# Kernel tuning notes

Hardware: AMD Instinct MI355X
Metric: run time of the kernel (lower is better)

## Reference

```python
import jax, jax.numpy as jnp
import numpy as np
from jax import lax

BETA = 0.9   # membrane decay
THR = 1.0    # firing threshold (soft reset)
K = 10       # number of time bins
# spatial pyramid for original_shape=(100,368) under 4 stride-2 SAME convs
HW = [(50, 184), (25, 92), (13, 46), (7, 23)]
CH = [4, 8, 16, 32]


def conv(x, w, b, stride=1):
    y = lax.conv_general_dilated(x, w, (stride, stride), 'SAME',
                                 dimension_numbers=('NCHW', 'OIHW', 'NCHW'))
    return y + b[None, :, None, None]


def spike(u):
    # heaviside forward, sigmoid straight-through surrogate backward
    s = (u > 0.0).astype(u.dtype)
    sg = jax.nn.sigmoid(4.0 * u)
    return sg + lax.stop_gradient(s - sg)


def setup_inputs() -> dict:
    key = jax.random.key(0)
    ks = jax.random.split(key, 12)
    T, B = 1000, 1
    x = jax.random.normal(ks[0], (T, B, 1, 100, 368), jnp.float32)

    def w(k, o, i, kh=3, kw=3):
        return 0.1 * jax.random.normal(k, (o, i, kh, kw), jnp.float32)

    inp = {'x': x}
    cin = [1] + CH[:3]
    for li in range(4):
        inp['w%d' % (li + 1)] = w(ks[1 + li], CH[li], cin[li])
        inp['b%d' % (li + 1)] = jnp.zeros((CH[li],), jnp.float32)
    sc = [2 * K * c for c in CH]  # skip channels: [80,160,320,640]
    inp['dw4'] = w(ks[5], 64, sc[3]); inp['db4'] = jnp.zeros((64,), jnp.float32)
    inp['dw3'] = w(ks[6], 32, 64 + sc[2]); inp['db3'] = jnp.zeros((32,), jnp.float32)
    inp['dw2'] = w(ks[7], 16, 32 + sc[1]); inp['db2'] = jnp.zeros((16,), jnp.float32)
    inp['dw1'] = w(ks[8], 8, 16 + sc[0]); inp['db1'] = jnp.zeros((8,), jnp.float32)
    inp['wo'] = w(ks[9], 1, 8, 1, 1); inp['bo'] = jnp.zeros((1,), jnp.float32)
    inp['total_steps'] = 1000
    inp['block_size'] = 100
    return inp


def reference(x, w1, b1, w2, b2, w3, b3, w4, b4,
              dw4, db4, dw3, db3, dw2, db2, dw1, db1, wo, bo,
              total_steps, block_size):
    S = total_steps // K  # steps per bin
    B = x.shape[1]
    xb = x.reshape((K, S) + x.shape[1:])  # [K,S,B,C,H,W]
    mems0 = tuple(jnp.zeros((B, CH[i], HW[i][0], HW[i][1]), x.dtype) for i in range(4))
    enc_w = [(w1, b1), (w2, b2), (w3, b3), (w4, b4)]

    def forward_step(x_t, mems):
        new_mems, spk = [], x_t
        for (wi, bi), m in zip(enc_w, mems):
            m = BETA * m + conv(spk, wi, bi, 2)
            spk = spike(m - THR)
            m = m - spk * THR  # soft reset
            new_mems.append(m)
        return tuple(new_mems)

    def step(carry, x_t):
        mems, sums, sqs = carry
        mems = forward_step(x_t, mems)
        sums = tuple(s + m for s, m in zip(sums, mems))
        sqs = tuple(q + m * m for q, m in zip(sqs, mems))
        return (mems, sums, sqs), None

    def bin_fn(mems, x_bin):
        zeros = tuple(jnp.zeros_like(m) for m in mems)
        (mems, sums, sqs), _ = lax.scan(step, (mems, zeros, zeros), x_bin)
        means = tuple(s / S for s in sums)
        stds = tuple(jnp.sqrt(jnp.maximum(q / S - mu * mu, 1e-8))
                     for q, mu in zip(sqs, means))
        return mems, (means, stds)

    _, (means, stds) = lax.scan(bin_fn, mems0, xb)  # each leaf: [K,B,C,H,W]

    def skip(mean, std):
        # torch.cat([mean0,std0,mean1,std1,...], dim=1) channel ordering
        f = jnp.stack([mean, std], axis=1)        # [K,2,B,C,H,W]
        f = jnp.transpose(f, (2, 0, 1, 3, 4, 5))  # [B,K,2,C,H,W]
        b_, k_, t_, c_, h_, w_ = f.shape
        return f.reshape(b_, k_ * t_ * c_, h_, w_)

    skips = [skip(means[i], stds[i]) for i in range(4)]

    def up(t, hw):
        return jax.image.resize(t, (t.shape[0], t.shape[1], hw[0], hw[1]), 'bilinear')

    relu = jax.nn.relu
    d = relu(conv(skips[3], dw4, db4))
    d = relu(conv(jnp.concatenate([up(d, HW[2]), skips[2]], 1), dw3, db3))
    d = relu(conv(jnp.concatenate([up(d, HW[1]), skips[1]], 1), dw2, db2))
    d = relu(conv(jnp.concatenate([up(d, HW[0]), skips[0]], 1), dw1, db1))
    tau_c = conv(up(d, (100, 368)), wo, bo)  # [B,1,100,368]
    return tau_c
```

## Files before the change

### kernel.cpp

```cpp
#include <hip/hip_runtime.h>

#define KBINS  10
#define SBIN   100
#define BETA   0.9f
#define THR    1.0f
#define CDIV(a,b) (((a)+(b)-1)/(b))


__global__ void k_zero16(float4* __restrict__ p, int n16) {
    int i = blockIdx.x * blockDim.x + threadIdx.x;
    if (i < n16) p[i] = make_float4(0.f, 0.f, 0.f, 0.f);
}

__global__ void k_conv1(const float* __restrict__ x,
                        const float* __restrict__ w1,
                        const float* __restrict__ b1,
                        float* __restrict__ c1, int tcount) {
    int n = blockIdx.x * blockDim.x + threadIdx.x;
    if (n >= tcount * 50 * 46) return;
    int wq  = n % 46;
    int tmp = n / 46;
    int h   = tmp % 50;
    int t   = tmp / 50;
    int w0  = wq * 4;

    const float* xt = x + (size_t)t * 36800;
    float rm2 = (h  < 49)  ? 1.f : 0.f;
    float cm8 = (w0 < 180) ? 1.f : 0.f;
    int   r2  = min(2 * h + 2, 99);
    int   cb  = 2 * w0;
    int   c8  = min(cb + 8, 367);

    const float* row0 = xt + (2 * h) * 368 + cb;
    const float* row1 = row0 + 368;
    const float* row2 = xt + r2 * 368 + cb;

    float tap[3][9];
    #pragma unroll
    for (int j = 0; j < 8; j++) {
        tap[0][j] = row0[j];
        tap[1][j] = row1[j];
        tap[2][j] = row2[j] * rm2;
    }
    tap[0][8] = xt[(2 * h) * 368 + c8] * cm8;
    tap[1][8] = xt[(2 * h + 1) * 368 + c8] * cm8;
    tap[2][8] = xt[r2 * 368 + c8] * (rm2 * cm8);

    float* ot = c1 + (size_t)t * 36800 + h * 184 + w0;
    #pragma unroll
    for (int co = 0; co < 4; co++) {
        float b = b1[co];
        float a0 = b, a1 = b, a2 = b, a3 = b;
        #pragma unroll
        for (int r = 0; r < 3; r++) {
            #pragma unroll
            for (int kw = 0; kw < 3; kw++) {
                float wv = w1[co * 9 + r * 3 + kw];
                a0 = fmaf(tap[r][0 + kw], wv, a0);
                a1 = fmaf(tap[r][2 + kw], wv, a1);
                a2 = fmaf(tap[r][4 + kw], wv, a2);
                a3 = fmaf(tap[r][6 + kw], wv, a3);
            }
        }
        *(float4*)(ot + (size_t)co * 9200) = make_float4(a0, a1, a2, a3);
    }
}

__global__ void k_scan(const float* __restrict__ cbuf,
                       unsigned char* __restrict__ spk,
                       float* __restrict__ skip,
                       float* __restrict__ mstate,
                       int C, int HW, int Win, int Wp, int HpWp,
                       int write_spk, int bin0, int nbins, int init) {
    const int PF = 20;
    int CHW = C * HW;
    int p = blockIdx.x * blockDim.x + threadIdx.x;
    if (p >= CHW) return;
    int c  = p / HW;
    int hw = p - c * HW;
    int h  = hw / Win, w = hw - h * Win;

    const size_t tstr = (size_t)C * HpWp;
    unsigned char* sp = spk + (size_t)bin0 * SBIN * tstr
                      + (size_t)c * HpWp + (h + 1) * Wp + (w + 1);

    float m = init ? 0.0f : mstate[p];
    float va[PF], vb[PF];
    #pragma unroll
    for (int j = 0; j < PF; j++) va[j] = cbuf[(size_t)j * CHW + p];

    const int T = nbins * SBIN;
    for (int k = 0; k < nbins; k++) {
        float s = 0.0f, q = 0.0f;
        for (int b = 0; b < SBIN / PF; b++) {
            int t0 = k * SBIN + b * PF;
            int tn = t0 + PF;
            bool more = (tn < T);
            #pragma unroll
            for (int j = 0; j < PF; j++)
                vb[j] = more ? cbuf[(size_t)(tn + j) * CHW + p] : 0.0f;
            #pragma unroll
            for (int j = 0; j < PF; j++) {
                m = fmaf(m, BETA, va[j]);
                float spv = (m - THR > 0.0f) ? 1.0f : 0.0f;
                m -= spv * THR;
                if (write_spk) sp[(size_t)(t0 + j) * tstr] = (unsigned char)spv;
                s += m;
                q = fmaf(m, m, q);
            }
            #pragma unroll
            for (int j = 0; j < PF; j++) va[j] = vb[j];
        }
        int g = bin0 + k;
        float mean = s * (1.0f / SBIN);
        float var  = q * (1.0f / SBIN) - mean * mean;
        float sd   = sqrtf(fmaxf(var, 1e-8f));
        skip[(size_t)(g * 2 * C + c) * HW + hw]     = mean;
        skip[(size_t)(g * 2 * C + C + c) * HW + hw] = sd;
    }
    mstate[p] = m;
}

template<int CIN, int COUT, int COG, int OW,
         int HOUT, int WOUT, int PADH, int HP, int WP>
__global__ void k_convs2(const unsigned char* __restrict__ spk,
                         const float* __restrict__ wt,
                         const float* __restrict__ bias,
                         float* __restrict__ out) {
    const int WQ = (WOUT + OW - 1) / OW;
    const int NT = 2 * OW + 1;
    int n = blockIdx.x * blockDim.x + threadIdx.x;
    if (n >= 1000 * HOUT * WQ) return;
    int wq  = n % WQ;
    int tmp = n / WQ;
    int h   = tmp % HOUT;
    int t   = tmp / HOUT;
    int cog = blockIdx.y;
    int w0  = wq * OW;

    const unsigned char* base = spk + (size_t)t * CIN * HP * WP
                              + (2 * h - PADH + 1) * WP + (2 * w0 + 1);

    float acc[OW][COG];
    #pragma unroll
    for (int q = 0; q < OW; q++)
        #pragma unroll
        for (int co = 0; co < COG; co++) acc[q][co] = bias[cog * COG + co];

    for (int ci = 0; ci < CIN; ci++) {
        const unsigned char* ic = base + (size_t)ci * HP * WP;
        float tap[3][NT];
        #pragma unroll
        for (int r = 0; r < 3; r++)
            #pragma unroll
            for (int j = 0; j < NT; j++)
                tap[r][j] = (float)ic[r * WP + j];
        #pragma unroll
        for (int co = 0; co < COG; co++) {
            const float* wc = wt + ((size_t)(cog * COG + co) * CIN + ci) * 9;
            #pragma unroll
            for (int r = 0; r < 3; r++)
                #pragma unroll
                for (int kw = 0; kw < 3; kw++) {
                    float wv = wc[r * 3 + kw];
                    #pragma unroll
                    for (int q = 0; q < OW; q++)
                        acc[q][co] = fmaf(tap[r][2 * q + kw], wv, acc[q][co]);
                }
        }
    }

    float* ot = out + ((size_t)t * COUT + cog * COG) * (HOUT * WOUT) + h * WOUT + w0;
    #pragma unroll
    for (int co = 0; co < COG; co++) {
        float* oc = ot + (size_t)co * (HOUT * WOUT);
        if constexpr (OW == 4) {
            *(float4*)oc = make_float4(acc[0][co], acc[1][co], acc[2][co], acc[3][co]);
        } else {
            if (w0 + 2 <= WOUT) *(float2*)oc = make_float2(acc[0][co], acc[1][co]);
            else                oc[0] = acc[0][co];
        }
    }
}

__global__ void k_up_cat(const float* __restrict__ up_src, int Cup, int Hi, int Wi,
                         const float* __restrict__ skip, int Cskip,
                         float* __restrict__ out, int Ho, int Wo) {
    int total = (Cup + Cskip) * Ho * Wo;
    int n = blockIdx.x * blockDim.x + threadIdx.x;
    if (n >= total) return;
    int w   = n % Wo;
    int tmp = n / Wo;
    int h   = tmp % Ho;
    int c   = tmp / Ho;
    float v;
    if (c < Cup) {
        float ph = (h + 0.5f) * (float)Hi / (float)Ho - 0.5f;
        float pw = (w + 0.5f) * (float)Wi / (float)Wo - 0.5f;
        float fh = floorf(ph), fw = floorf(pw);
        int h0 = (int)fh, w0 = (int)fw;
        float ah = ph - fh, aw = pw - fw;
        int h0c = min(max(h0, 0), Hi - 1), h1c = min(max(h0 + 1, 0), Hi - 1);
        int w0c = min(max(w0, 0), Wi - 1), w1c = min(max(w0 + 1, 0), Wi - 1);
        const float* sc = up_src + (size_t)c * Hi * Wi;
        float v00 = sc[h0c * Wi + w0c], v01 = sc[h0c * Wi + w1c];
        float v10 = sc[h1c * Wi + w0c], v11 = sc[h1c * Wi + w1c];
        v = (1.0f - ah) * ((1.0f - aw) * v00 + aw * v01)
          + ah * ((1.0f - aw) * v10 + aw * v11);
    } else {
        v = skip[(size_t)(c - Cup) * Ho * Wo + h * Wo + w];
    }
    out[n] = v;
}

template<int CIN, int CS, int COG>
__global__ void k_dconv(const float* __restrict__ in,
                        const float* __restrict__ wt,
                        float* __restrict__ part,
                        int Cout, int H, int W) {
    int HW  = H * W;
    int pix = blockIdx.x * blockDim.x + threadIdx.x;
    if (pix >= HW) return;
    int co0   = blockIdx.y * COG;
    int chunk = blockIdx.z;
    int h = pix / W, w = pix - h * W;

    int off[9]; float msk[9];
    #pragma unroll
    for (int kh = 0; kh < 3; kh++) {
        int r = h + kh - 1;
        bool rok = (r >= 0) && (r < H);
        int rc = rok ? r : 0;
        #pragma unroll
        for (int kw = 0; kw < 3; kw++) {
            int cc = w + kw - 1;
            bool cok = (cc >= 0) && (cc < W);
            int ccc = cok ? cc : 0;
            off[kh * 3 + kw] = rc * W + ccc;
            msk[kh * 3 + kw] = (rok && cok) ? 1.0f : 0.0f;
        }
    }

    const float* ibase = in + (size_t)chunk * CS * HW;
    const float* wbase = wt + ((size_t)co0 * CIN + (size_t)chunk * CS) * 9;

    float acc[COG];
    #pragma unroll
    for (int co = 0; co < COG; co++) acc[co] = 0.0f;

    #pragma unroll 8
    for (int ci = 0; ci < CS; ci++) {
        const float* ic = ibase + (size_t)ci * HW;
        float tap[9];
        #pragma unroll
        for (int j = 0; j < 9; j++)
            tap[j] = msk[j] * ic[off[j]];
        #pragma unroll
        for (int co = 0; co < COG; co++) {
            const float* wc = wbase + ((size_t)co * CIN + ci) * 9;
            #pragma unroll
            for (int j = 0; j < 9; j++)
                acc[co] = fmaf(tap[j], wc[j], acc[co]);
        }
    }

    float* pp = part + ((size_t)chunk * Cout + co0) * HW + pix;
    #pragma unroll
    for (int co = 0; co < COG; co++) pp[(size_t)co * HW] = acc[co];
}

__global__ void k_reduce_relu(const float* __restrict__ part,
                              const float* __restrict__ bias,
                              float* __restrict__ out,
                              int Cout, int HW, int nchunks) {
    int n = blockIdx.x * blockDim.x + threadIdx.x;
    if (n >= Cout * HW) return;
    int co = n / HW;
    float acc = bias[co];
    for (int c = 0; c < nchunks; c++)
        acc += part[(size_t)c * Cout * HW + n];
    out[n] = fmaxf(acc, 0.0f);
}

__global__ void k_final(const float* __restrict__ d1,
                        const float* __restrict__ wo,
                        const float* __restrict__ bo,
                        float* __restrict__ out) {
    int n = blockIdx.x * blockDim.x + threadIdx.x;
    if (n >= 36800) return;
    int w = n % 368, h = n / 368;
    float ph = (h + 0.5f) * 0.5f - 0.5f;
    float pw = (w + 0.5f) * 0.5f - 0.5f;
    float fh = floorf(ph), fw = floorf(pw);
    int h0 = (int)fh, w0 = (int)fw;
    float ah = ph - fh, aw = pw - fw;
    int h0c = min(max(h0, 0), 49),  h1c = min(max(h0 + 1, 0), 49);
    int w0c = min(max(w0, 0), 183), w1c = min(max(w0 + 1, 0), 183);
    float acc = bo[0];
    #pragma unroll
    for (int c = 0; c < 8; c++) {
        const float* sc = d1 + c * 9200;
        float v00 = sc[h0c * 184 + w0c], v01 = sc[h0c * 184 + w1c];
        float v10 = sc[h1c * 184 + w0c], v11 = sc[h1c * 184 + w1c];
        float v = (1.0f - ah) * ((1.0f - aw) * v00 + aw * v01)
                + ah * ((1.0f - aw) * v10 + aw * v11);
        acc = fmaf(wo[c], v, acc);
    }
    out[n] = acc;
}

extern "C" void kernel_launch(void* const* d_in, const int* in_sizes, int n_in,
                              void* d_out, int out_size, void* d_ws, size_t ws_size,
                              hipStream_t stream) {
    (void)in_sizes; (void)n_in; (void)out_size; (void)ws_size;
    const float* x   = (const float*)d_in[0];
    const float* w1  = (const float*)d_in[1];
    const float* b1  = (const float*)d_in[2];
    const float* w2  = (const float*)d_in[3];
    const float* b2  = (const float*)d_in[4];
    const float* w3  = (const float*)d_in[5];
    const float* b3  = (const float*)d_in[6];
    const float* w4  = (const float*)d_in[7];
    const float* b4  = (const float*)d_in[8];
    const float* dw4 = (const float*)d_in[9];
    const float* db4 = (const float*)d_in[10];
    const float* dw3 = (const float*)d_in[11];
    const float* db3 = (const float*)d_in[12];
    const float* dw2 = (const float*)d_in[13];
    const float* db2 = (const float*)d_in[14];
    const float* dw1 = (const float*)d_in[15];
    const float* db1 = (const float*)d_in[16];
    const float* wo  = (const float*)d_in[17];
    const float* bo  = (const float*)d_in[18];
    float* out = (float*)d_out;

    char* ws = (char*)d_ws;
    size_t off = 0;
    auto alloc = [&](size_t bytes) -> void* {
        void* p = ws + off;
        off += (bytes + 255) & ~(size_t)255;
        return p;
    };
    float* cbuf = (float*)alloc(73600000);
    unsigned char* spk1r = (unsigned char*)alloc(39936000 + 256);
    unsigned char* spk2r = (unsigned char*)alloc(21600000 + 256);
    unsigned char* spk3r = (unsigned char*)alloc(12960000 + 256);
    unsigned char* spk1p = spk1r + 63;
    unsigned char* spk2p = spk2r + 63;
    unsigned char* spk3p = spk3r + 63;
    float* skip0 = (float*)alloc(2944000);
    float* skip1 = (float*)alloc(1472000);
    float* skip2 = (float*)alloc(765440);
    float* skip3 = (float*)alloc(412160);
    float* msS   = (float*)alloc(147200);
    char* dec = (char*)cbuf;
    size_t doff = 0;
    auto dalloc = [&](size_t bytes) -> void* {
        void* p = dec + doff;
        doff += (bytes + 255) & ~(size_t)255;
        return p;
    };
    float* d4   = (float*)dalloc(10304u * 4);
    float* d3   = (float*)dalloc(19136u * 4);
    float* d2   = (float*)dalloc(36800u * 4);
    float* d1   = (float*)dalloc(73600u * 4);
    float* cat3 = (float*)dalloc(229632u * 4);
    float* cat2 = (float*)dalloc(441600u * 4);
    float* cat1 = (float*)dalloc(883200u * 4);
    float* part = (float*)dalloc(230400u * 4);

    const int BS  = 256;
    const int SBS = 64;

    {
        size_t nb = (39936000 + 256) + (21600000 + 256) + (12960000 + 256);
        int n16 = (int)(nb / 16);
        k_zero16<<<CDIV(n16, BS), BS, 0, stream>>>((float4*)spk1r, n16);
    }

    for (int q = 0; q < 2; q++) {
        k_conv1<<<CDIV(500 * 50 * 46, BS), BS, 0, stream>>>(
            x + (size_t)q * 500 * 36800, w1, b1, cbuf, 500);
        k_scan<<<CDIV(36800, SBS), SBS, 0, stream>>>(
            cbuf, spk1p, skip0, msS, 4, 9200, 184, 192, 52 * 192,
            1, 5 * q, 5, (q == 0) ? 1 : 0);
    }

    k_convs2<4, 8, 8, 4, 25, 92, 0, 52, 192>
        <<<dim3(CDIV(1000 * 25 * 23, BS), 1), BS, 0, stream>>>(spk1p, w2, b2, cbuf);
    k_scan<<<CDIV(18400, SBS), SBS, 0, stream>>>(cbuf, spk2p, skip1, msS,
                                                 8, 2300, 92, 100, 27 * 100, 1, 0, 10, 1);

    k_convs2<8, 16, 16, 2, 13, 46, 1, 27, 100>
        <<<dim3(CDIV(1000 * 13 * 23, BS), 1), BS, 0, stream>>>(spk2p, w3, b3, cbuf);
    k_scan<<<CDIV(9568, SBS), SBS, 0, stream>>>(cbuf, spk3p, skip2, msS,
                                                16, 598, 46, 54, 15 * 54, 1, 0, 10, 1);

    k_convs2<16, 32, 16, 2, 7, 23, 1, 15, 54>
        <<<dim3(CDIV(1000 * 7 * 12, BS), 2), BS, 0, stream>>>(spk3p, w4, b4, cbuf);
    k_scan<<<CDIV(5152, SBS), SBS, 0, stream>>>(cbuf, spk1p , skip3, msS,
                                                32, 161, 23, 31, 9 * 31, 0, 0, 10, 1);

    {
        dim3 g(CDIV(161, 64), 16, 20);
        k_dconv<640, 32, 4><<<g, 64, 0, stream>>>(skip3, dw4, part, 64, 7, 23);
        k_reduce_relu<<<CDIV(64 * 161, BS), BS, 0, stream>>>(part, db4, d4, 64, 161, 20);
    }
    {
        k_up_cat<<<CDIV(384 * 598, BS), BS, 0, stream>>>(d4, 64, 7, 23,
                                                         skip2, 320, cat3, 13, 46);
        dim3 g(CDIV(598, 64), 8, 12);
        k_dconv<384, 32, 4><<<g, 64, 0, stream>>>(cat3, dw3, part, 32, 13, 46);
        k_reduce_relu<<<CDIV(32 * 598, BS), BS, 0, stream>>>(part, db3, d3, 32, 598, 12);
    }
    {
        k_up_cat<<<CDIV(192 * 2300, BS), BS, 0, stream>>>(d3, 32, 13, 46,
                                                          skip1, 160, cat2, 25, 92);
        dim3 g(CDIV(2300, 128), 4, 6);
        k_dconv<192, 32, 4><<<g, 128, 0, stream>>>(cat2, dw2, part, 16, 25, 92);
        k_reduce_relu<<<CDIV(16 * 2300, BS), BS, 0, stream>>>(part, db2, d2, 16, 2300, 6);
    }
    {
        k_up_cat<<<CDIV(96 * 9200, BS), BS, 0, stream>>>(d2, 16, 25, 92,
                                                         skip0, 80, cat1, 50, 184);
        dim3 g(CDIV(9200, BS), 2, 3);
        k_dconv<96, 32, 4><<<g, BS, 0, stream>>>(cat1, dw1, part, 8, 50, 184);
        k_reduce_relu<<<CDIV(8 * 9200, BS), BS, 0, stream>>>(part, db1, d1, 8, 9200, 3);
    }
    k_final<<<CDIV(36800, BS), BS, 0, stream>>>(d1, wo, bo, out);
}
```

Baseline: 837.3 us.

## Fuse decoder reduce, relu and upsample; read skips directly without concat buffers

The decoder no longer builds concatenated up-sample/skip buffers. A new conv kernel picks its input chunk from either the up-sampled tensor or the skip tensor. The partial-sum reduction, bias, ReLU and bilinear upsample are merged into one kernel, and the last reduce is folded into the final 1x1 output kernel. This removes several launches and the full-resolution concat copies, but each output pixel now re-reduces four neighbouring partial sums instead of one.

```diff
diff --git a/kernel.cpp b/kernel.cpp
--- a/kernel.cpp
+++ b/kernel.cpp
@@ -183,36 +183,6 @@
     }
 }
 
-__global__ void k_up_cat(const float* __restrict__ up_src, int Cup, int Hi, int Wi,
-                         const float* __restrict__ skip, int Cskip,
-                         float* __restrict__ out, int Ho, int Wo) {
-    int total = (Cup + Cskip) * Ho * Wo;
-    int n = blockIdx.x * blockDim.x + threadIdx.x;
-    if (n >= total) return;
-    int w   = n % Wo;
-    int tmp = n / Wo;
-    int h   = tmp % Ho;
-    int c   = tmp / Ho;
-    float v;
-    if (c < Cup) {
-        float ph = (h + 0.5f) * (float)Hi / (float)Ho - 0.5f;
-        float pw = (w + 0.5f) * (float)Wi / (float)Wo - 0.5f;
-        float fh = floorf(ph), fw = floorf(pw);
-        int h0 = (int)fh, w0 = (int)fw;
-        float ah = ph - fh, aw = pw - fw;
-        int h0c = min(max(h0, 0), Hi - 1), h1c = min(max(h0 + 1, 0), Hi - 1);
-        int w0c = min(max(w0, 0), Wi - 1), w1c = min(max(w0 + 1, 0), Wi - 1);
-        const float* sc = up_src + (size_t)c * Hi * Wi;
-        float v00 = sc[h0c * Wi + w0c], v01 = sc[h0c * Wi + w1c];
-        float v10 = sc[h1c * Wi + w0c], v11 = sc[h1c * Wi + w1c];
-        v = (1.0f - ah) * ((1.0f - aw) * v00 + aw * v01)
-          + ah * ((1.0f - aw) * v10 + aw * v11);
-    } else {
-        v = skip[(size_t)(c - Cup) * Ho * Wo + h * Wo + w];
-    }
-    out[n] = v;
-}
-
 template<int CIN, int CS, int COG>
 __global__ void k_dconv(const float* __restrict__ in,
                         const float* __restrict__ wt,
@@ -269,43 +239,137 @@
     for (int co = 0; co < COG; co++) pp[(size_t)co * HW] = acc[co];
 }
 
-__global__ void k_reduce_relu(const float* __restrict__ part,
-                              const float* __restrict__ bias,
-                              float* __restrict__ out,
-                              int Cout, int HW, int nchunks) {
+template<int CIN, int CS, int COG>
+__global__ void k_dconv2(const float* __restrict__ ubuf, int Cup,
+                         const float* __restrict__ skp,
+                         const float* __restrict__ wt,
+                         float* __restrict__ part,
+                         int Cout, int H, int W, int upChunks) {
+    int HW  = H * W;
+    int pix = blockIdx.x * blockDim.x + threadIdx.x;
+    if (pix >= HW) return;
+    int co0   = blockIdx.y * COG;
+    int chunk = blockIdx.z;
+    int h = pix / W, w = pix - h * W;
+
+    int off[9]; float msk[9];
+    #pragma unroll
+    for (int kh = 0; kh < 3; kh++) {
+        int r = h + kh - 1;
+        bool rok = (r >= 0) && (r < H);
+        int rc = rok ? r : 0;
+        #pragma unroll
+        for (int kw = 0; kw < 3; kw++) {
+            int cc = w + kw - 1;
+            bool cok = (cc >= 0) && (cc < W);
+            int ccc = cok ? cc : 0;
+            off[kh * 3 + kw] = rc * W + ccc;
+            msk[kh * 3 + kw] = (rok && cok) ? 1.0f : 0.0f;
+        }
+    }
+
+    const float* ibase = (chunk < upChunks)
+        ? ubuf + (size_t)chunk * CS * HW
+        : skp  + ((size_t)chunk * CS - Cup) * HW;
+    const float* wbase = wt + ((size_t)co0 * CIN + (size_t)chunk * CS) * 9;
+
+    float acc[COG];
+    #pragma unroll
+    for (int co = 0; co < COG; co++) acc[co] = 0.0f;
+
+    #pragma unroll 8
+    for (int ci = 0; ci < CS; ci++) {
+        const float* ic = ibase + (size_t)ci * HW;
+        float tap[9];
+        #pragma unroll
+        for (int j = 0; j < 9; j++)
+            tap[j] = msk[j] * ic[off[j]];
+        #pragma unroll
+        for (int co = 0; co < COG; co++) {
+            const float* wc = wbase + ((size_t)co * CIN + ci) * 9;
+            #pragma unroll
+            for (int j = 0; j < 9; j++)
+                acc[co] = fmaf(tap[j], wc[j], acc[co]);
+        }
+    }
+
+    float* pp = part + ((size_t)chunk * Cout + co0) * HW + pix;
+    #pragma unroll
+    for (int co = 0; co < COG; co++) pp[(size_t)co * HW] = acc[co];
+}
+
+__global__ void k_reduce_up(const float* __restrict__ part,
+                            const float* __restrict__ bias,
+                            float* __restrict__ ubuf,
+                            int C, int Hi, int Wi, int Ho, int Wo, int nchunks) {
+    int total = C * Ho * Wo;
     int n = blockIdx.x * blockDim.x + threadIdx.x;
-    if (n >= Cout * HW) return;
-    int co = n / HW;
-    float acc = bias[co];
-    for (int c = 0; c < nchunks; c++)
-        acc += part[(size_t)c * Cout * HW + n];
-    out[n] = fmaxf(acc, 0.0f);
-}
-
-__global__ void k_final(const float* __restrict__ d1,
-                        const float* __restrict__ wo,
-                        const float* __restrict__ bo,
-                        float* __restrict__ out) {
+    if (n >= total) return;
+    int wo_ = n % Wo;
+    int tmp = n / Wo;
+    int ho  = tmp % Ho;
+    int c   = tmp / Ho;
+
+    float ph = (ho + 0.5f) * (float)Hi / (float)Ho - 0.5f;
+    float pw = (wo_ + 0.5f) * (float)Wi / (float)Wo - 0.5f;
+    float fh = floorf(ph), fw = floorf(pw);
+    float ah = ph - fh, aw = pw - fw;
+    int h0 = (int)fh, w0 = (int)fw;
+    int h0c = min(max(h0, 0), Hi - 1), h1c = min(max(h0 + 1, 0), Hi - 1);
+    int w0c = min(max(w0, 0), Wi - 1), w1c = min(max(w0 + 1, 0), Wi - 1);
+
+    int HWi = Hi * Wi;
+    float b = bias[c];
+    int p00 = h0c * Wi + w0c, p01 = h0c * Wi + w1c;
+    int p10 = h1c * Wi + w0c, p11 = h1c * Wi + w1c;
+    float a00 = b, a01 = b, a10 = b, a11 = b;
+    const float* pc = part + (size_t)c * HWi;
+    #pragma unroll 4
+    for (int k = 0; k < nchunks; k++) {
+        const float* pk = pc + (size_t)k * C * HWi;
+        a00 += pk[p00]; a01 += pk[p01]; a10 += pk[p10]; a11 += pk[p11];
+    }
+    a00 = fmaxf(a00, 0.f); a01 = fmaxf(a01, 0.f);
+    a10 = fmaxf(a10, 0.f); a11 = fmaxf(a11, 0.f);
+    ubuf[n] = (1.0f - ah) * ((1.0f - aw) * a00 + aw * a01)
+            + ah * ((1.0f - aw) * a10 + aw * a11);
+}
+
+__global__ void k_final_f(const float* __restrict__ part,
+                          const float* __restrict__ db,
+                          const float* __restrict__ wo,
+                          const float* __restrict__ bo,
+                          float* __restrict__ out, int nchunks) {
     int n = blockIdx.x * blockDim.x + threadIdx.x;
     if (n >= 36800) return;
     int w = n % 368, h = n / 368;
     float ph = (h + 0.5f) * 0.5f - 0.5f;
     float pw = (w + 0.5f) * 0.5f - 0.5f;
     float fh = floorf(ph), fw = floorf(pw);
+    float ah = ph - fh, aw = pw - fw;
     int h0 = (int)fh, w0 = (int)fw;
-    float ah = ph - fh, aw = pw - fw;
     int h0c = min(max(h0, 0), 49),  h1c = min(max(h0 + 1, 0), 49);
     int w0c = min(max(w0, 0), 183), w1c = min(max(w0 + 1, 0), 183);
+    int p00 = h0c * 184 + w0c, p01 = h0c * 184 + w1c;
+    int p10 = h1c * 184 + w0c, p11 = h1c * 184 + w1c;
+
     float acc = bo[0];
     #pragma unroll
     for (int c = 0; c < 8; c++) {
-        const float* sc = d1 + c * 9200;
-        float v00 = sc[h0c * 184 + w0c], v01 = sc[h0c * 184 + w1c];
-        float v10 = sc[h1c * 184 + w0c], v11 = sc[h1c * 184 + w1c];
-        float v = (1.0f - ah) * ((1.0f - aw) * v00 + aw * v01)
-                + ah * ((1.0f - aw) * v10 + aw * v11);
+        float b = db[c];
+        float a00 = b, a01 = b, a10 = b, a11 = b;
+        const float* pc = part + (size_t)c * 9200;
+        for (int k = 0; k < 6; k++) {
+            const float* pk = pc + (size_t)k * 8 * 9200;
+            a00 += pk[p00]; a01 += pk[p01]; a10 += pk[p10]; a11 += pk[p11];
+        }
+        a00 = fmaxf(a00, 0.f); a01 = fmaxf(a01, 0.f);
+        a10 = fmaxf(a10, 0.f); a11 = fmaxf(a11, 0.f);
+        float v = (1.0f - ah) * ((1.0f - aw) * a00 + aw * a01)
+                + ah * ((1.0f - aw) * a10 + aw * a11);
         acc = fmaf(wo[c], v, acc);
     }
+    (void)nchunks;
     out[n] = acc;
 }
 
@@ -360,14 +424,10 @@
         doff += (bytes + 255) & ~(size_t)255;
         return p;
     };
-    float* d4   = (float*)dalloc(10304u * 4);
-    float* d3   = (float*)dalloc(19136u * 4);
-    float* d2   = (float*)dalloc(36800u * 4);
-    float* d1   = (float*)dalloc(73600u * 4);
-    float* cat3 = (float*)dalloc(229632u * 4);
-    float* cat2 = (float*)dalloc(441600u * 4);
-    float* cat1 = (float*)dalloc(883200u * 4);
-    float* part = (float*)dalloc(230400u * 4);
+    float* part = (float*)dalloc(450000u * 4);
+    float* u4   = (float*)dalloc(38272u * 4);
+    float* u3   = (float*)dalloc(73600u * 4);
+    float* u2   = (float*)dalloc(147200u * 4);
 
     const int BS  = 256;
     const int SBS = 64;
@@ -404,28 +464,27 @@
     {
         dim3 g(CDIV(161, 64), 16, 20);
         k_dconv<640, 32, 4><<<g, 64, 0, stream>>>(skip3, dw4, part, 64, 7, 23);
-        k_reduce_relu<<<CDIV(64 * 161, BS), BS, 0, stream>>>(part, db4, d4, 64, 161, 20);
+        k_reduce_up<<<CDIV(64 * 598, BS), BS, 0, stream>>>(part, db4, u4,
+                                                           64, 7, 23, 13, 46, 20);
     }
     {
-        k_up_cat<<<CDIV(384 * 598, BS), BS, 0, stream>>>(d4, 64, 7, 23,
-                                                         skip2, 320, cat3, 13, 46);
         dim3 g(CDIV(598, 64), 8, 12);
-        k_dconv<384, 32, 4><<<g, 64, 0, stream>>>(cat3, dw3, part, 32, 13, 46);
-        k_reduce_relu<<<CDIV(32 * 598, BS), BS, 0, stream>>>(part, db3, d3, 32, 598, 12);
+        k_dconv2<384, 32, 4><<<g, 64, 0, stream>>>(u4, 64, skip2, dw3, part,
+                                                   32, 13, 46, 2);
+        k_reduce_up<<<CDIV(32 * 2300, BS), BS, 0, stream>>>(part, db3, u3,
+                                                            32, 13, 46, 25, 92, 12);
     }
     {
-        k_up_cat<<<CDIV(192 * 2300, BS), BS, 0, stream>>>(d3, 32, 13, 46,
-                                                          skip1, 160, cat2, 25, 92);
         dim3 g(CDIV(2300, 128), 4, 6);
-        k_dconv<192, 32, 4><<<g, 128, 0, stream>>>(cat2, dw2, part, 16, 25, 92);
-        k_reduce_relu<<<CDIV(16 * 2300, BS), BS, 0, stream>>>(part, db2, d2, 16, 2300, 6);
+        k_dconv2<192, 32, 4><<<g, 128, 0, stream>>>(u3, 32, skip1, dw2, part,
+                                                    16, 25, 92, 1);
+        k_reduce_up<<<CDIV(16 * 9200, BS), BS, 0, stream>>>(part, db2, u2,
+                                                            16, 25, 92, 50, 184, 6);
     }
     {
-        k_up_cat<<<CDIV(96 * 9200, BS), BS, 0, stream>>>(d2, 16, 25, 92,
-                                                         skip0, 80, cat1, 50, 184);
-        dim3 g(CDIV(9200, BS), 2, 3);
-        k_dconv<96, 32, 4><<<g, BS, 0, stream>>>(cat1, dw1, part, 8, 50, 184);
-        k_reduce_relu<<<CDIV(8 * 9200, BS), BS, 0, stream>>>(part, db1, d1, 8, 9200, 3);
-    }
-    k_final<<<CDIV(36800, BS), BS, 0, stream>>>(d1, wo, bo, out);
-}
+        dim3 g(CDIV(9200, BS), 2, 6);
+        k_dconv2<96, 16, 4><<<g, BS, 0, stream>>>(u2, 16, skip0, dw1, part,
+                                                  8, 50, 184, 1);
+    }
+    k_final_f<<<CDIV(36800, BS), BS, 0, stream>>>(part, db1, wo, bo, out, 6);
+}
```

Result: slower. 855.8 us (+2.2%).
